# Optimization experiments

Measured on AMD Instinct MI355X. Metric: run time of the kernel, lower is better.

The kernel has to match this reference:

```python
import jax, jax.numpy as jnp
import numpy as np

B, T, IN_DIM, HID = 8, 1024, 32, 512
L = 2                       # num_layers
DI = 2 * HID                # d_inner (expand=2)
DS = 16                     # d_state
K = 4                       # d_conv
DTR = HID // 16             # dt_rank = ceil(d_model/16)
F = 96                      # forecast_len


def setup_inputs() -> dict:
    key = jax.random.key(0)
    ks = jax.random.split(key, 10)
    nrm = lambda k, shape, scale: jax.random.normal(k, shape, jnp.float32) * scale
    x = jax.random.normal(ks[0], (B, T, IN_DIM), jnp.float32)
    ip_w = nrm(ks[1], (HID, IN_DIM), IN_DIM ** -0.5)
    ip_b = jnp.zeros((HID,), jnp.float32)
    norm_w = jnp.ones((L, HID), jnp.float32)
    inp_w = nrm(ks[2], (L, 2 * DI, HID), HID ** -0.5)
    conv_w = nrm(ks[3], (L, DI, 1, K), K ** -0.5)
    conv_b = jnp.zeros((L, DI), jnp.float32)
    xproj_w = nrm(ks[4], (L, DTR + 2 * DS, DI), DI ** -0.5)
    dtproj_w = nrm(ks[5], (L, DI, DTR), DTR ** -0.5)
    dtproj_b = nrm(ks[6], (L, DI), 0.5) - 4.0  # softplus -> small positive dt
    # S4D-real init: A = -[1..d_state], stored as A_log
    A_log = jnp.log(jnp.broadcast_to(jnp.arange(1, DS + 1, dtype=jnp.float32), (L, DI, DS)))
    D = jnp.ones((L, DI), jnp.float32)
    outp_w = nrm(ks[7], (L, HID, DI), DI ** -0.5)
    fc_w = nrm(ks[8], (F, HID), HID ** -0.5)
    fc_b = jnp.zeros((F,), jnp.float32)
    return dict(x=x, ip_w=ip_w, ip_b=ip_b, norm_w=norm_w, inp_w=inp_w,
                conv_w=conv_w, conv_b=conv_b, xproj_w=xproj_w,
                dtproj_w=dtproj_w, dtproj_b=dtproj_b, A_log=A_log, D=D,
                outp_w=outp_w, fc_w=fc_w, fc_b=fc_b)


def _rmsnorm(h, w, eps=1e-5):
    return h * jax.lax.rsqrt(jnp.mean(h * h, axis=-1, keepdims=True) + eps) * w


def _mamba_block(h, inp_w, conv_w, conv_b, xproj_w, dtproj_w, dtproj_b, A_log, Dp, outp_w):
    Bsz = h.shape[0]
    xz = jnp.einsum('btd,ed->bte', h, inp_w)            # (B,T,2*DI)
    x_in, z = jnp.split(xz, 2, axis=-1)
    # causal depthwise conv1d over time
    xc = jnp.transpose(x_in, (0, 2, 1))                 # (B,DI,T)
    xc = jax.lax.conv_general_dilated(
        xc, conv_w, window_strides=(1,), padding=[(K - 1, 0)],
        feature_group_count=DI, dimension_numbers=('NCH', 'OIH', 'NCH'))
    xc = xc + conv_b[None, :, None]
    x_ssm = jax.nn.silu(jnp.transpose(xc, (0, 2, 1)))   # (B,T,DI)
    dbl = jnp.einsum('btd,ed->bte', x_ssm, xproj_w)     # (B,T,DTR+2*DS)
    dt_raw = dbl[..., :DTR]
    Bm = dbl[..., DTR:DTR + DS]                          # (B,T,DS)
    Cm = dbl[..., DTR + DS:]                             # (B,T,DS)
    delta = jax.nn.softplus(jnp.einsum('btr,dr->btd', dt_raw, dtproj_w) + dtproj_b)
    A = -jnp.exp(A_log)                                  # (DI,DS)

    def step(hst, inp):
        dt_t, B_t, C_t, x_t = inp                        # (B,DI),(B,DS),(B,DS),(B,DI)
        dA = jnp.exp(dt_t[:, :, None] * A)               # (B,DI,DS)
        hst = hst * dA + dt_t[:, :, None] * B_t[:, None, :] * x_t[:, :, None]
        y_t = jnp.einsum('bds,bs->bd', hst, C_t)
        return hst, y_t

    h0 = jnp.zeros((Bsz, DI, DS), dtype=h.dtype)
    xs = (jnp.moveaxis(delta, 1, 0), jnp.moveaxis(Bm, 1, 0),
          jnp.moveaxis(Cm, 1, 0), jnp.moveaxis(x_ssm, 1, 0))
    _, ys = jax.lax.scan(step, h0, xs)                   # ys: (T,B,DI)
    y = jnp.moveaxis(ys, 0, 1) + x_ssm * Dp
    y = y * jax.nn.silu(z)
    return jnp.einsum('btd,ed->bte', y, outp_w)


def reference(x, ip_w, ip_b, norm_w, inp_w, conv_w, conv_b, xproj_w,
              dtproj_w, dtproj_b, A_log, D, outp_w, fc_w, fc_b):
    coeff = jnp.array([0.3, 0.5, 0.9, 1.0], dtype=x.dtype)
    x = x.at[:, :, :4].multiply(coeff)
    h = jnp.einsum('bti,hi->bth', x, ip_w) + ip_b        # (B,T,HID)
    for l in range(L):
        h = h + _mamba_block(_rmsnorm(h, norm_w[l]), inp_w[l], conv_w[l],
                             conv_b[l], xproj_w[l], dtproj_w[l], dtproj_b[l],
                             A_log[l], D[l], outp_w[l])
    last = h[:, -1, :]
    return last @ fc_w.T + fc_b                          # (B,F)
```

## Files before the change

### kernel.cpp

```cpp
#include <hip/hip_runtime.h>
#include <math.h>

#define NB   8
#define NT   1024
#define NIN  32
#define NH   512
#define NL   2
#define NDI  1024
#define NDS  16
#define NK   4
#define NDTR 32
#define NF   96
#define NBT  (NB*NT)
#define NE2  (2*NDI)
#define NC   32
#define TC   (NT/NC)

typedef __attribute__((ext_vector_type(8))) short  short8;
typedef __attribute__((ext_vector_type(8))) __bf16 bf16x8;
typedef __attribute__((ext_vector_type(4))) float  f32x4;

__device__ inline void bsplit(float a, short& hi, short& lo) {
  unsigned u = __float_as_uint(a);
  unsigned r = (u + 0x7fffu + ((u >> 16) & 1u)) & 0xffff0000u;
  hi = (short)(r >> 16);
  float res = a - __uint_as_float(r);
  unsigned u2 = __float_as_uint(res);
  lo = (short)((u2 + 0x7fffu + ((u2 >> 16) & 1u)) >> 16);
}

__device__ inline f32x4 mfma_bf16(short8 a, short8 b, f32x4 c) {
  union Cast { short8 s; bf16x8 h; };
  Cast ca, cb; ca.s = a; cb.s = b;
  return __builtin_amdgcn_mfma_f32_16x16x32_bf16(ca.h, cb.h, c, 0, 0, 0);
}

__device__ inline void gld_lds16(const short* g, short* l) {
  __builtin_amdgcn_global_load_lds(
      (const __attribute__((address_space(1))) unsigned int*)g,
      (__attribute__((address_space(3))) unsigned int*)l, 16, 0, 0);
}

__global__ __launch_bounds__(256) void k_input_proj(
    const float* __restrict__ x, const float* __restrict__ ip_w,
    const float* __restrict__ ip_b, float* __restrict__ h) {
  __shared__ float xt[NIN][65];
  __shared__ float wt[NIN][132];
  int tid = threadIdx.x;
  int r0 = blockIdx.x * 64, c0 = blockIdx.y * 128;
  #pragma unroll
  for (int it = 0; it < 2; it++) {
    int i = tid + it*256;
    int row = i >> 3, seg = i & 7;
    float4 v = *(const float4*)&x[(size_t)(r0+row)*NIN + seg*4];
    if (seg == 0) { v.x *= 0.3f; v.y *= 0.5f; v.z *= 0.9f; }
    xt[seg*4+0][row] = v.x; xt[seg*4+1][row] = v.y;
    xt[seg*4+2][row] = v.z; xt[seg*4+3][row] = v.w;
  }
  #pragma unroll
  for (int it = 0; it < 4; it++) {
    int i = tid + it*256;
    int col = i >> 3, seg = i & 7;
    float4 v = *(const float4*)&ip_w[(size_t)(c0+col)*NIN + seg*4];
    wt[seg*4+0][col] = v.x; wt[seg*4+1][col] = v.y;
    wt[seg*4+2][col] = v.z; wt[seg*4+3][col] = v.w;
  }
  __syncthreads();
  int tx = tid & 31, ty = tid >> 5;
  float acc[8][4];
  #pragma unroll
  for (int i = 0; i < 8; i++)
    #pragma unroll
    for (int j = 0; j < 4; j++) acc[i][j] = 0.f;
  #pragma unroll
  for (int k = 0; k < NIN; k++) {
    float4 w4 = *(const float4*)&wt[k][tx*4];
    #pragma unroll
    for (int i = 0; i < 8; i++) {
      float a = xt[k][ty + 8*i];
      acc[i][0] = fmaf(a, w4.x, acc[i][0]);
      acc[i][1] = fmaf(a, w4.y, acc[i][1]);
      acc[i][2] = fmaf(a, w4.z, acc[i][2]);
      acc[i][3] = fmaf(a, w4.w, acc[i][3]);
    }
  }
  float4 bias = *(const float4*)&ip_b[c0 + tx*4];
  #pragma unroll
  for (int i = 0; i < 8; i++) {
    float4 o = make_float4(acc[i][0]+bias.x, acc[i][1]+bias.y,
                           acc[i][2]+bias.z, acc[i][3]+bias.w);
    *(float4*)&h[(size_t)(r0 + ty + 8*i)*NH + c0 + tx*4] = o;
  }
}

__global__ __launch_bounds__(256) void k_rms_split(
    const float* __restrict__ h, const float* __restrict__ nw,
    short* __restrict__ oh, short* __restrict__ ol) {
  int row = blockIdx.x, tid = threadIdx.x;
  float2 v = *(const float2*)&h[(size_t)row*NH + tid*2];
  float ss = v.x*v.x + v.y*v.y;
  #pragma unroll
  for (int off = 32; off > 0; off >>= 1) ss += __shfl_down(ss, off, 64);
  __shared__ float red[4];
  __shared__ float sc_sh;
  if ((tid & 63) == 0) red[tid >> 6] = ss;
  __syncthreads();
  if (tid == 0) sc_sh = rsqrtf((red[0]+red[1]+red[2]+red[3]) * (1.0f/NH) + 1e-5f);
  __syncthreads();
  float sc = sc_sh;
  float2 w2 = *(const float2*)&nw[tid*2];
  short h0,l0,h1,l1;
  bsplit(v.x*sc*w2.x, h0, l0);
  bsplit(v.y*sc*w2.y, h1, l1);
  ushort2 hh; hh.x=(unsigned short)h0; hh.y=(unsigned short)h1;
  ushort2 ll; ll.x=(unsigned short)l0; ll.y=(unsigned short)l1;
  *(ushort2*)&oh[(size_t)row*NH + tid*2] = hh;
  *(ushort2*)&ol[(size_t)row*NH + tid*2] = ll;
}

__global__ __launch_bounds__(256) void k_split_w(
    const float* __restrict__ W, short* __restrict__ wh, short* __restrict__ wl) {
  int i = (blockIdx.x*256 + threadIdx.x) * 8;
  float4 a = *(const float4*)&W[i];
  float4 b = *(const float4*)&W[i+4];
  float v[8] = {a.x,a.y,a.z,a.w,b.x,b.y,b.z,b.w};
  short8 H, L;
  #pragma unroll
  for (int j = 0; j < 8; j++) { short hi, lo; bsplit(v[j], hi, lo); H[j] = hi; L[j] = lo; }
  *(short8*)&wh[i] = H;
  *(short8*)&wl[i] = L;
}

__global__ __launch_bounds__(256) void k_gemm_b3(
    const short* __restrict__ Ah, const short* __restrict__ Al,
    const short* __restrict__ Bh, const short* __restrict__ Bl,
    float* __restrict__ C, int M, int N, int Kd, int accum) {
  __shared__ short lAh[4096], lAl[4096], lBh[4096], lBl[4096];
  int tid = threadIdx.x;
  int lane = tid & 63, w = tid >> 6;
  int m = lane & 15, q = lane >> 4;
  int bm = blockIdx.x * 128, bn = blockIdx.y * 128;
  int wm = (w & 1) * 64, wn = (w >> 1) * 64;
  int s = q ^ ((m >> 1) & 3);
  int ca = ((wm + m) * 4 + s) * 8;
  int cb = ((wn + m) * 4 + s) * 8;

  int r0 = tid >> 2,        s0 = (tid & 3) ^ ((r0 >> 1) & 3);
  int c1 = 256 + tid, r1 = c1 >> 2, s1 = (c1 & 3) ^ ((r1 >> 1) & 3);
  const short* gAh0 = Ah + (size_t)(bm + r0) * Kd + s0 * 8;
  const short* gAh1 = Ah + (size_t)(bm + r1) * Kd + s1 * 8;
  const short* gAl0 = Al + (size_t)(bm + r0) * Kd + s0 * 8;
  const short* gAl1 = Al + (size_t)(bm + r1) * Kd + s1 * 8;
  const short* gBh0 = Bh + (size_t)(bn + r0) * Kd + s0 * 8;
  const short* gBh1 = Bh + (size_t)(bn + r1) * Kd + s1 * 8;
  const short* gBl0 = Bl + (size_t)(bn + r0) * Kd + s0 * 8;
  const short* gBl1 = Bl + (size_t)(bn + r1) * Kd + s1 * 8;
  int ld0 = (tid & ~63) * 8;
  int ld1 = 2048 + ld0;

  f32x4 acc[4][4];
  #pragma unroll
  for (int i = 0; i < 4; i++)
    #pragma unroll
    for (int j = 0; j < 4; j++) acc[i][j] = (f32x4)0.f;

  for (int k0 = 0; k0 < Kd; k0 += 32) {
    __syncthreads();
    gld_lds16(gAh0 + k0, lAh + ld0); gld_lds16(gAh1 + k0, lAh + ld1);
    gld_lds16(gAl0 + k0, lAl + ld0); gld_lds16(gAl1 + k0, lAl + ld1);
    gld_lds16(gBh0 + k0, lBh + ld0); gld_lds16(gBh1 + k0, lBh + ld1);
    gld_lds16(gBl0 + k0, lBl + ld0); gld_lds16(gBl1 + k0, lBl + ld1);
    __syncthreads();
    short8 fAh[4], fAl[4];
    #pragma unroll
    for (int mt = 0; mt < 4; mt++) {
      fAh[mt] = *(const short8*)&lAh[ca + mt*512];
      fAl[mt] = *(const short8*)&lAl[ca + mt*512];
    }
    #pragma unroll
    for (int nt = 0; nt < 4; nt++) {
      short8 fBh = *(const short8*)&lBh[cb + nt*512];
      short8 fBl = *(const short8*)&lBl[cb + nt*512];
      #pragma unroll
      for (int mt = 0; mt < 4; mt++) {
        acc[mt][nt] = mfma_bf16(fAh[mt], fBh, acc[mt][nt]);
        acc[mt][nt] = mfma_bf16(fAl[mt], fBh, acc[mt][nt]);
        acc[mt][nt] = mfma_bf16(fAh[mt], fBl, acc[mt][nt]);
      }
    }
  }
  __syncthreads();
  float* tile = ((float*)lAh) + w * 320;
  int rr = lane >> 2, cc2 = (lane & 3) * 4;
  #pragma unroll
  for (int mt = 0; mt < 4; mt++) {
    #pragma unroll
    for (int nt = 0; nt < 4; nt++) {
      f32x4 v = acc[mt][nt];
      #pragma unroll
      for (int r2 = 0; r2 < 4; r2++) tile[(q*4+r2)*20 + m] = v[r2];
      __builtin_amdgcn_wave_barrier();
      f32x4 o = *(const f32x4*)&tile[rr*20 + cc2];
      __builtin_amdgcn_wave_barrier();
      size_t gi = (size_t)(bm + wm + mt*16 + rr) * N + (bn + wn + nt*16 + cc2);
      if (accum) {
        f32x4 old = *(const f32x4*)&C[gi];
        o.x += old.x; o.y += old.y; o.z += old.z; o.w += old.w;
      }
      *(f32x4*)&C[gi] = o;
    }
  }
}

__global__ __launch_bounds__(256) void k_conv_silu(
    const float* __restrict__ xz, const float* __restrict__ cw,
    const float* __restrict__ cb, float* __restrict__ xs) {
  int idx = blockIdx.x*256 + threadIdx.x;
  int d = idx & (NDI-1);
  int row = idx >> 10;
  int t = row & (NT-1);
  const float* base = xz + (size_t)row*NE2 + d;
  float4 w = *(const float4*)(cw + d*NK);
  float acc = cb[d] + w.w * base[0];
  if (t >= 1) acc += w.z * base[-(ptrdiff_t)NE2];
  if (t >= 2) acc += w.y * base[-2*(ptrdiff_t)NE2];
  if (t >= 3) acc += w.x * base[-3*(ptrdiff_t)NE2];
  xs[idx] = acc / (1.0f + expf(-acc));
}

__global__ __launch_bounds__(256) void k_xproj(
    const float* __restrict__ xs, const float* __restrict__ xw,
    float* __restrict__ dbl) {
  __shared__ float As[64][36];
  __shared__ float Bs[64][68];
  int tid = threadIdx.x;
  int r0 = blockIdx.x * 32;
  int tx = tid & 15, ty = tid >> 4;
  float acc[2][4];
  #pragma unroll
  for (int i = 0; i < 2; i++)
    #pragma unroll
    for (int j = 0; j < 4; j++) acc[i][j] = 0.f;

  for (int k0 = 0; k0 < NDI; k0 += 64) {
    __syncthreads();
    #pragma unroll
    for (int it = 0; it < 2; it++) {
      int i = tid + it*256;
      int row = i >> 4, seg = i & 15;
      float4 v = *(const float4*)&xs[(size_t)(r0+row)*NDI + k0 + seg*4];
      As[seg*4+0][row] = v.x; As[seg*4+1][row] = v.y;
      As[seg*4+2][row] = v.z; As[seg*4+3][row] = v.w;
    }
    #pragma unroll
    for (int it = 0; it < 4; it++) {
      int i = tid + it*256;
      int row = i >> 4, seg = i & 15;
      float4 v = *(const float4*)&xw[(size_t)row*NDI + k0 + seg*4];
      Bs[seg*4+0][row] = v.x; Bs[seg*4+1][row] = v.y;
      Bs[seg*4+2][row] = v.z; Bs[seg*4+3][row] = v.w;
    }
    __syncthreads();
    #pragma unroll
    for (int k = 0; k < 64; k++) {
      float2 a2 = *(const float2*)&As[k][ty*2];
      float4 b4 = *(const float4*)&Bs[k][tx*4];
      acc[0][0]=fmaf(a2.x,b4.x,acc[0][0]); acc[0][1]=fmaf(a2.x,b4.y,acc[0][1]);
      acc[0][2]=fmaf(a2.x,b4.z,acc[0][2]); acc[0][3]=fmaf(a2.x,b4.w,acc[0][3]);
      acc[1][0]=fmaf(a2.y,b4.x,acc[1][0]); acc[1][1]=fmaf(a2.y,b4.y,acc[1][1]);
      acc[1][2]=fmaf(a2.y,b4.z,acc[1][2]); acc[1][3]=fmaf(a2.y,b4.w,acc[1][3]);
    }
  }
  #pragma unroll
  for (int i = 0; i < 2; i++) {
    float4 v = make_float4(acc[i][0], acc[i][1], acc[i][2], acc[i][3]);
    *(float4*)&dbl[(size_t)(r0 + ty*2 + i)*64 + tx*4] = v;
  }
}

__global__ __launch_bounds__(256) void k_dtproj(
    const float* __restrict__ dbl, const float* __restrict__ dtw,
    const float* __restrict__ dtb, float* __restrict__ dly) {
  __shared__ float As[32][68];
  __shared__ float Bs[32][68];
  int tid = threadIdx.x;
  int r0 = blockIdx.x * 64, c0 = blockIdx.y * 64;
  int tx = tid & 15, ty = tid >> 4;
  {
    #pragma unroll
    for (int it = 0; it < 2; it++) {
      int i = tid + it*256;
      int row = i >> 3, seg = i & 7;
      float4 v = *(const float4*)&dbl[(size_t)(r0+row)*64 + seg*4];
      As[seg*4+0][row] = v.x; As[seg*4+1][row] = v.y;
      As[seg*4+2][row] = v.z; As[seg*4+3][row] = v.w;
      float4 u = *(const float4*)&dtw[(size_t)(c0+row)*NDTR + seg*4];
      Bs[seg*4+0][row] = u.x; Bs[seg*4+1][row] = u.y;
      Bs[seg*4+2][row] = u.z; Bs[seg*4+3][row] = u.w;
    }
  }
  __syncthreads();
  float acc[4][4];
  #pragma unroll
  for (int i = 0; i < 4; i++)
    #pragma unroll
    for (int j = 0; j < 4; j++) acc[i][j] = 0.f;
  #pragma unroll
  for (int k = 0; k < 32; k++) {
    float4 a4 = *(const float4*)&As[k][ty*4];
    float4 b4 = *(const float4*)&Bs[k][tx*4];
    acc[0][0]=fmaf(a4.x,b4.x,acc[0][0]); acc[0][1]=fmaf(a4.x,b4.y,acc[0][1]);
    acc[0][2]=fmaf(a4.x,b4.z,acc[0][2]); acc[0][3]=fmaf(a4.x,b4.w,acc[0][3]);
    acc[1][0]=fmaf(a4.y,b4.x,acc[1][0]); acc[1][1]=fmaf(a4.y,b4.y,acc[1][1]);
    acc[1][2]=fmaf(a4.y,b4.z,acc[1][2]); acc[1][3]=fmaf(a4.y,b4.w,acc[1][3]);
    acc[2][0]=fmaf(a4.z,b4.x,acc[2][0]); acc[2][1]=fmaf(a4.z,b4.y,acc[2][1]);
    acc[2][2]=fmaf(a4.z,b4.z,acc[2][2]); acc[2][3]=fmaf(a4.z,b4.w,acc[2][3]);
    acc[3][0]=fmaf(a4.w,b4.x,acc[3][0]); acc[3][1]=fmaf(a4.w,b4.y,acc[3][1]);
    acc[3][2]=fmaf(a4.w,b4.z,acc[3][2]); acc[3][3]=fmaf(a4.w,b4.w,acc[3][3]);
  }
  float4 bias = *(const float4*)&dtb[c0 + tx*4];
  #pragma unroll
  for (int i = 0; i < 4; i++) {
    float v[4] = {acc[i][0]+bias.x, acc[i][1]+bias.y, acc[i][2]+bias.z, acc[i][3]+bias.w};
    float4 o;
    o.x = fmaxf(v[0],0.f) + log1pf(expf(-fabsf(v[0])));
    o.y = fmaxf(v[1],0.f) + log1pf(expf(-fabsf(v[1])));
    o.z = fmaxf(v[2],0.f) + log1pf(expf(-fabsf(v[2])));
    o.w = fmaxf(v[3],0.f) + log1pf(expf(-fabsf(v[3])));
    *(float4*)&dly[(size_t)(r0 + ty*4 + i)*NDI + c0 + tx*4] = o;
  }
}

__global__ __launch_bounds__(256) void k_scan_chunk(
    const float* __restrict__ dly, const float* __restrict__ xs,
    const float* __restrict__ dbl, const float* __restrict__ A_log,
    float* __restrict__ aprod, float* __restrict__ hend) {
  int bx = blockIdx.x;
  int c    = bx & (NC-1);
  int dblk = (bx >> 5) & 3;
  int b    = bx >> 7;
  int d = (dblk << 8) + threadIdx.x;
  float a[NDS], ap[NDS], h[NDS];
  #pragma unroll
  for (int s = 0; s < NDS; s++) {
    a[s] = -expf(A_log[d*NDS + s]);
    ap[s] = 1.f; h[s] = 0.f;
  }
  size_t row0 = (size_t)b*NT + (size_t)c*TC;
  for (int t = 0; t < TC; t++) {
    size_t r = row0 + t;
    float dl = dly[r*NDI + d];
    float xv = xs[r*NDI + d];
    float bc[NDS];
    #pragma unroll
    for (int i = 0; i < NDS; i++) bc[i] = dbl[r*64 + 32 + i];
    float dlx = dl * xv;
    #pragma unroll
    for (int s = 0; s < NDS; s++) {
      float dA = __expf(dl * a[s]);
      ap[s] *= dA;
      h[s] = fmaf(h[s], dA, dlx * bc[s]);
    }
  }
  size_t o = (((size_t)b*NC + c)*NDI + d)*NDS;
  #pragma unroll
  for (int s = 0; s < NDS; s += 4) {
    *(float4*)&aprod[o + s] = make_float4(ap[s], ap[s+1], ap[s+2], ap[s+3]);
    *(float4*)&hend [o + s] = make_float4(h[s],  h[s+1],  h[s+2],  h[s+3]);
  }
}

__global__ __launch_bounds__(256) void k_scan_combine(
    const float* __restrict__ aprod, const float* __restrict__ hend,
    float* __restrict__ hinit) {
  int idx = blockIdx.x*256 + threadIdx.x;
  int b  = idx >> 14;
  int ds = idx & 16383;
  float hcur = 0.f;
  for (int c = 0; c < NC; c++) {
    size_t o = (((size_t)b*NC + c) << 14) + ds;
    hinit[o] = hcur;
    hcur = fmaf(aprod[o], hcur, hend[o]);
  }
}

__global__ __launch_bounds__(256) void k_scan_emit(
    const float* __restrict__ dly, const float* __restrict__ xs,
    const float* __restrict__ xz, const float* __restrict__ dbl,
    const float* __restrict__ A_log, const float* __restrict__ Dp,
    const float* __restrict__ hinit,
    short* __restrict__ yhp, short* __restrict__ ylp) {
  int bx = blockIdx.x;
  int c    = bx & (NC-1);
  int dblk = (bx >> 5) & 3;
  int b    = bx >> 7;
  int d = (dblk << 8) + threadIdx.x;
  float a[NDS], h[NDS];
  size_t o = (((size_t)b*NC + c)*NDI + d)*NDS;
  #pragma unroll
  for (int s = 0; s < NDS; s++) {
    a[s] = -expf(A_log[d*NDS + s]);
    h[s] = hinit[o + s];
  }
  float Dd = Dp[d];
  size_t row0 = (size_t)b*NT + (size_t)c*TC;

  float dl_n = dly[row0*NDI + d];
  float xv_n = xs[row0*NDI + d];
  float zv_n = xz[row0*NE2 + NDI + d];
  for (int t = 0; t < TC; t++) {
    size_t r = row0 + t;
    float dl = dl_n, xv = xv_n, zv = zv_n;
    float bc[32];
    #pragma unroll
    for (int i = 0; i < 32; i++) bc[i] = dbl[r*64 + 32 + i];
    if (t + 1 < TC) {
      dl_n = dly[(r+1)*NDI + d];
      xv_n = xs[(r+1)*NDI + d];
      zv_n = xz[(r+1)*NE2 + NDI + d];
    }
    float dlx = dl * xv;
    float y = 0.f;
    #pragma unroll
    for (int s = 0; s < NDS; s++) {
      float dA = __expf(dl * a[s]);
      h[s] = fmaf(h[s], dA, dlx * bc[s]);
      y = fmaf(h[s], bc[16 + s], y);
    }
    y = (y + xv*Dd) * (zv / (1.0f + __expf(-zv)));
    short yh, yl; bsplit(y, yh, yl);
    yhp[r*NDI + d] = yh;
    ylp[r*NDI + d] = yl;
  }
}

__global__ __launch_bounds__(96) void k_fc(
    const float* __restrict__ h, const float* __restrict__ fc_w,
    const float* __restrict__ fc_b, float* __restrict__ out) {
  int b = blockIdx.x, f = threadIdx.x;
  __shared__ float hr[NH];
  for (int i = f; i < NH; i += NF) hr[i] = h[((size_t)b*NT + (NT-1))*NH + i];
  __syncthreads();
  const float4* wp = (const float4*)(fc_w + (size_t)f*NH);
  float acc = fc_b[f];
  for (int i = 0; i < NH/4; i++) {
    float4 w4 = wp[i];
    acc += hr[i*4+0]*w4.x + hr[i*4+1]*w4.y + hr[i*4+2]*w4.z + hr[i*4+3]*w4.w;
  }
  out[b*NF + f] = acc;
}

extern "C" void kernel_launch(void* const* d_in, const int* in_sizes, int n_in,
                              void* d_out, int out_size, void* d_ws, size_t ws_size,
                              hipStream_t stream) {
  (void)in_sizes; (void)n_in; (void)out_size; (void)ws_size;
  const float* x        = (const float*)d_in[0];
  const float* ip_w     = (const float*)d_in[1];
  const float* ip_b     = (const float*)d_in[2];
  const float* norm_w   = (const float*)d_in[3];
  const float* inp_w    = (const float*)d_in[4];
  const float* conv_w   = (const float*)d_in[5];
  const float* conv_b   = (const float*)d_in[6];
  const float* xproj_w  = (const float*)d_in[7];
  const float* dtproj_w = (const float*)d_in[8];
  const float* dtproj_b = (const float*)d_in[9];
  const float* A_log    = (const float*)d_in[10];
  const float* Dv       = (const float*)d_in[11];
  const float* outp_w   = (const float*)d_in[12];
  const float* fc_w     = (const float*)d_in[13];
  const float* fc_b     = (const float*)d_in[14];
  float* out = (float*)d_out;

  float* ws    = (float*)d_ws;
  float* h     = ws;
  float* xzb   = h     + 4194304;
  float* xs    = xzb   + 16777216;
  float* dblb  = xs    + 8388608;
  float* dly   = dblb  + 524288;
  float* aprod = dly   + 8388608;
  float* hend  = aprod + 4194304;
  float* hinit = hend  + 4194304;
  short* w1h   = (short*)(hinit + 4194304);
  short* w1l   = w1h + 1048576;
  short* w2h   = w1l + 1048576;
  short* w2l   = w2h + 524288;
  short* a1h   = (short*)dly;
  short* a1l   = a1h + 4194304;
  short* yh    = (short*)aprod;
  short* yl    = (short*)hend;

  k_input_proj<<<dim3(NBT/64, NH/128), 256, 0, stream>>>(x, ip_w, ip_b, h);
  for (int l = 0; l < NL; l++) {
    k_rms_split<<<NBT, 256, 0, stream>>>(h, norm_w + l*NH, a1h, a1l);
    k_split_w<<<(NE2*NH)/(256*8), 256, 0, stream>>>(inp_w + (size_t)l*NE2*NH, w1h, w1l);
    k_gemm_b3<<<dim3(NBT/128, NE2/128), 256, 0, stream>>>(
        a1h, a1l, w1h, w1l, xzb, NBT, NE2, NH, 0);
    k_conv_silu<<<(NBT*NDI)/256, 256, 0, stream>>>(
        xzb, conv_w + l*NDI*NK, conv_b + l*NDI, xs);
    k_xproj<<<NBT/32, 256, 0, stream>>>(xs, xproj_w + (size_t)l*64*NDI, dblb);
    k_dtproj<<<dim3(NBT/64, NDI/64), 256, 0, stream>>>(
        dblb, dtproj_w + (size_t)l*NDI*NDTR, dtproj_b + l*NDI, dly);
    k_scan_chunk<<<NB*4*NC, 256, 0, stream>>>(
        dly, xs, dblb, A_log + (size_t)l*NDI*NDS, aprod, hend);
    k_scan_combine<<<(NB*NDI*NDS)/256, 256, 0, stream>>>(aprod, hend, hinit);
    k_scan_emit<<<NB*4*NC, 256, 0, stream>>>(
        dly, xs, xzb, dblb, A_log + (size_t)l*NDI*NDS, Dv + l*NDI, hinit, yh, yl);
    k_split_w<<<(NH*NDI)/(256*8), 256, 0, stream>>>(outp_w + (size_t)l*NH*NDI, w2h, w2l);
    k_gemm_b3<<<dim3(NBT/128, NH/128), 256, 0, stream>>>(
        yh, yl, w2h, w2l, h, NBT, NH, NDI, 1);
  }
  k_fc<<<NB, NF, 0, stream>>>(h, fc_w, fc_b, out);
}
```

Measured before the change: 707.7 us.

## Fuse conv+SiLU into x_proj and recompute dt projection inside scan kernels

The depthwise causal conv and SiLU now run inside the x_proj GEMM kernel, loading a haloed xz tile into shared memory and writing xs as a side output. The separate dt_proj kernel and its 32 MB delta buffer are removed; both scan kernels recompute delta per step from the dt-rank columns of dbl with per-thread dt weights held in registers, plus softplus. Weight splitting for both layers is hoisted out of the layer loop into two launches. This cuts launches and a large activation round trip through memory, at the cost of more register pressure and repeated dt math (done in both scan passes).

```diff
diff --git a/kernel.cpp b/kernel.cpp
--- a/kernel.cpp
+++ b/kernel.cpp
@@ -212,29 +212,16 @@
   }
 }
 
-__global__ __launch_bounds__(256) void k_conv_silu(
+__global__ __launch_bounds__(256) void k_convxproj(
     const float* __restrict__ xz, const float* __restrict__ cw,
-    const float* __restrict__ cb, float* __restrict__ xs) {
-  int idx = blockIdx.x*256 + threadIdx.x;
-  int d = idx & (NDI-1);
-  int row = idx >> 10;
-  int t = row & (NT-1);
-  const float* base = xz + (size_t)row*NE2 + d;
-  float4 w = *(const float4*)(cw + d*NK);
-  float acc = cb[d] + w.w * base[0];
-  if (t >= 1) acc += w.z * base[-(ptrdiff_t)NE2];
-  if (t >= 2) acc += w.y * base[-2*(ptrdiff_t)NE2];
-  if (t >= 3) acc += w.x * base[-3*(ptrdiff_t)NE2];
-  xs[idx] = acc / (1.0f + expf(-acc));
-}
-
-__global__ __launch_bounds__(256) void k_xproj(
-    const float* __restrict__ xs, const float* __restrict__ xw,
-    float* __restrict__ dbl) {
-  __shared__ float As[64][36];
+    const float* __restrict__ cb, const float* __restrict__ xw,
+    float* __restrict__ xs, float* __restrict__ dbl) {
+  __shared__ float xin[35*68];
+  __shared__ float As[64*33];
   __shared__ float Bs[64][68];
   int tid = threadIdx.x;
   int r0 = blockIdx.x * 32;
+  int t0 = r0 & (NT-1);
   int tx = tid & 15, ty = tid >> 4;
   float acc[2][4];
   #pragma unroll
@@ -245,12 +232,15 @@
   for (int k0 = 0; k0 < NDI; k0 += 64) {
     __syncthreads();
     #pragma unroll
-    for (int it = 0; it < 2; it++) {
+    for (int it = 0; it < 3; it++) {
       int i = tid + it*256;
-      int row = i >> 4, seg = i & 15;
-      float4 v = *(const float4*)&xs[(size_t)(r0+row)*NDI + k0 + seg*4];
-      As[seg*4+0][row] = v.x; As[seg*4+1][row] = v.y;
-      As[seg*4+2][row] = v.z; As[seg*4+3][row] = v.w;
+      if (i < 560) {
+        int row = i >> 4, seg = i & 15;
+        float4 v;
+        if (t0 == 0 && row < 3) v = make_float4(0.f, 0.f, 0.f, 0.f);
+        else v = *(const float4*)&xz[(size_t)(r0 - 3 + row)*NE2 + k0 + seg*4];
+        *(float4*)&xin[row*68 + seg*4] = v;
+      }
     }
     #pragma unroll
     for (int it = 0; it < 4; it++) {
@@ -262,13 +252,29 @@
     }
     __syncthreads();
     #pragma unroll
+    for (int it = 0; it < 8; it++) {
+      int i = tid + it*256;
+      int row = i >> 6, c = i & 63;
+      float4 w = *(const float4*)&cw[(k0 + c)*NK];
+      float v = cb[k0 + c]
+              + w.w * xin[(row+3)*68 + c]
+              + w.z * xin[(row+2)*68 + c]
+              + w.y * xin[(row+1)*68 + c]
+              + w.x * xin[(row+0)*68 + c];
+      v = v / (1.0f + expf(-v));
+      As[c*33 + row] = v;
+      xs[(size_t)(r0 + row)*NDI + k0 + c] = v;
+    }
+    __syncthreads();
+    #pragma unroll
     for (int k = 0; k < 64; k++) {
-      float2 a2 = *(const float2*)&As[k][ty*2];
+      float a0 = As[k*33 + ty*2];
+      float a1 = As[k*33 + ty*2 + 1];
       float4 b4 = *(const float4*)&Bs[k][tx*4];
-      acc[0][0]=fmaf(a2.x,b4.x,acc[0][0]); acc[0][1]=fmaf(a2.x,b4.y,acc[0][1]);
-      acc[0][2]=fmaf(a2.x,b4.z,acc[0][2]); acc[0][3]=fmaf(a2.x,b4.w,acc[0][3]);
-      acc[1][0]=fmaf(a2.y,b4.x,acc[1][0]); acc[1][1]=fmaf(a2.y,b4.y,acc[1][1]);
-      acc[1][2]=fmaf(a2.y,b4.z,acc[1][2]); acc[1][3]=fmaf(a2.y,b4.w,acc[1][3]);
+      acc[0][0]=fmaf(a0,b4.x,acc[0][0]); acc[0][1]=fmaf(a0,b4.y,acc[0][1]);
+      acc[0][2]=fmaf(a0,b4.z,acc[0][2]); acc[0][3]=fmaf(a0,b4.w,acc[0][3]);
+      acc[1][0]=fmaf(a1,b4.x,acc[1][0]); acc[1][1]=fmaf(a1,b4.y,acc[1][1]);
+      acc[1][2]=fmaf(a1,b4.z,acc[1][2]); acc[1][3]=fmaf(a1,b4.w,acc[1][3]);
     }
   }
   #pragma unroll
@@ -278,88 +284,44 @@
   }
 }
 
-__global__ __launch_bounds__(256) void k_dtproj(
-    const float* __restrict__ dbl, const float* __restrict__ dtw,
-    const float* __restrict__ dtb, float* __restrict__ dly) {
-  __shared__ float As[32][68];
-  __shared__ float Bs[32][68];
-  int tid = threadIdx.x;
-  int r0 = blockIdx.x * 64, c0 = blockIdx.y * 64;
-  int tx = tid & 15, ty = tid >> 4;
-  {
-    #pragma unroll
-    for (int it = 0; it < 2; it++) {
-      int i = tid + it*256;
-      int row = i >> 3, seg = i & 7;
-      float4 v = *(const float4*)&dbl[(size_t)(r0+row)*64 + seg*4];
-      As[seg*4+0][row] = v.x; As[seg*4+1][row] = v.y;
-      As[seg*4+2][row] = v.z; As[seg*4+3][row] = v.w;
-      float4 u = *(const float4*)&dtw[(size_t)(c0+row)*NDTR + seg*4];
-      Bs[seg*4+0][row] = u.x; Bs[seg*4+1][row] = u.y;
-      Bs[seg*4+2][row] = u.z; Bs[seg*4+3][row] = u.w;
-    }
-  }
-  __syncthreads();
-  float acc[4][4];
-  #pragma unroll
-  for (int i = 0; i < 4; i++)
-    #pragma unroll
-    for (int j = 0; j < 4; j++) acc[i][j] = 0.f;
-  #pragma unroll
-  for (int k = 0; k < 32; k++) {
-    float4 a4 = *(const float4*)&As[k][ty*4];
-    float4 b4 = *(const float4*)&Bs[k][tx*4];
-    acc[0][0]=fmaf(a4.x,b4.x,acc[0][0]); acc[0][1]=fmaf(a4.x,b4.y,acc[0][1]);
-    acc[0][2]=fmaf(a4.x,b4.z,acc[0][2]); acc[0][3]=fmaf(a4.x,b4.w,acc[0][3]);
-    acc[1][0]=fmaf(a4.y,b4.x,acc[1][0]); acc[1][1]=fmaf(a4.y,b4.y,acc[1][1]);
-    acc[1][2]=fmaf(a4.y,b4.z,acc[1][2]); acc[1][3]=fmaf(a4.y,b4.w,acc[1][3]);
-    acc[2][0]=fmaf(a4.z,b4.x,acc[2][0]); acc[2][1]=fmaf(a4.z,b4.y,acc[2][1]);
-    acc[2][2]=fmaf(a4.z,b4.z,acc[2][2]); acc[2][3]=fmaf(a4.z,b4.w,acc[2][3]);
-    acc[3][0]=fmaf(a4.w,b4.x,acc[3][0]); acc[3][1]=fmaf(a4.w,b4.y,acc[3][1]);
-    acc[3][2]=fmaf(a4.w,b4.z,acc[3][2]); acc[3][3]=fmaf(a4.w,b4.w,acc[3][3]);
-  }
-  float4 bias = *(const float4*)&dtb[c0 + tx*4];
-  #pragma unroll
-  for (int i = 0; i < 4; i++) {
-    float v[4] = {acc[i][0]+bias.x, acc[i][1]+bias.y, acc[i][2]+bias.z, acc[i][3]+bias.w};
-    float4 o;
-    o.x = fmaxf(v[0],0.f) + log1pf(expf(-fabsf(v[0])));
-    o.y = fmaxf(v[1],0.f) + log1pf(expf(-fabsf(v[1])));
-    o.z = fmaxf(v[2],0.f) + log1pf(expf(-fabsf(v[2])));
-    o.w = fmaxf(v[3],0.f) + log1pf(expf(-fabsf(v[3])));
-    *(float4*)&dly[(size_t)(r0 + ty*4 + i)*NDI + c0 + tx*4] = o;
-  }
-}
-
 __global__ __launch_bounds__(256) void k_scan_chunk(
-    const float* __restrict__ dly, const float* __restrict__ xs,
-    const float* __restrict__ dbl, const float* __restrict__ A_log,
+    const float* __restrict__ xs, const float* __restrict__ dbl,
+    const float* __restrict__ dtw, const float* __restrict__ dtb,
+    const float* __restrict__ A_log,
     float* __restrict__ aprod, float* __restrict__ hend) {
   int bx = blockIdx.x;
   int c    = bx & (NC-1);
   int dblk = (bx >> 5) & 3;
   int b    = bx >> 7;
   int d = (dblk << 8) + threadIdx.x;
-  float a[NDS], ap[NDS], h[NDS];
+  float a[NDS], ap[NDS], h[NDS], wr[NDTR];
   #pragma unroll
   for (int s = 0; s < NDS; s++) {
     a[s] = -expf(A_log[d*NDS + s]);
     ap[s] = 1.f; h[s] = 0.f;
   }
+  #pragma unroll
+  for (int k = 0; k < NDTR; k++) wr[k] = dtw[d*NDTR + k];
+  float bias = dtb[d];
   size_t row0 = (size_t)b*NT + (size_t)c*TC;
+  float xv_n = xs[row0*NDI + d];
   for (int t = 0; t < TC; t++) {
     size_t r = row0 + t;
-    float dl = dly[r*NDI + d];
-    float xv = xs[r*NDI + d];
-    float bc[NDS];
-    #pragma unroll
-    for (int i = 0; i < NDS; i++) bc[i] = dbl[r*64 + 32 + i];
+    float raw[48];
+    #pragma unroll
+    for (int i = 0; i < 48; i++) raw[i] = dbl[r*64 + i];
+    float xv = xv_n;
+    if (t + 1 < TC) xv_n = xs[(r+1)*NDI + d];
+    float acc = bias;
+    #pragma unroll
+    for (int k = 0; k < NDTR; k++) acc = fmaf(raw[k], wr[k], acc);
+    float dl = fmaxf(acc, 0.f) + log1pf(expf(-fabsf(acc)));
     float dlx = dl * xv;
     #pragma unroll
     for (int s = 0; s < NDS; s++) {
       float dA = __expf(dl * a[s]);
       ap[s] *= dA;
-      h[s] = fmaf(h[s], dA, dlx * bc[s]);
+      h[s] = fmaf(h[s], dA, dlx * raw[32 + s]);
     }
   }
   size_t o = (((size_t)b*NC + c)*NDI + d)*NDS;
@@ -385,8 +347,9 @@
 }
 
 __global__ __launch_bounds__(256) void k_scan_emit(
-    const float* __restrict__ dly, const float* __restrict__ xs,
-    const float* __restrict__ xz, const float* __restrict__ dbl,
+    const float* __restrict__ xs, const float* __restrict__ xz,
+    const float* __restrict__ dbl,
+    const float* __restrict__ dtw, const float* __restrict__ dtb,
     const float* __restrict__ A_log, const float* __restrict__ Dp,
     const float* __restrict__ hinit,
     short* __restrict__ yhp, short* __restrict__ ylp) {
@@ -395,37 +358,42 @@
   int dblk = (bx >> 5) & 3;
   int b    = bx >> 7;
   int d = (dblk << 8) + threadIdx.x;
-  float a[NDS], h[NDS];
+  float a[NDS], h[NDS], wr[NDTR];
   size_t o = (((size_t)b*NC + c)*NDI + d)*NDS;
   #pragma unroll
   for (int s = 0; s < NDS; s++) {
     a[s] = -expf(A_log[d*NDS + s]);
     h[s] = hinit[o + s];
   }
+  #pragma unroll
+  for (int k = 0; k < NDTR; k++) wr[k] = dtw[d*NDTR + k];
+  float bias = dtb[d];
   float Dd = Dp[d];
   size_t row0 = (size_t)b*NT + (size_t)c*TC;
 
-  float dl_n = dly[row0*NDI + d];
   float xv_n = xs[row0*NDI + d];
   float zv_n = xz[row0*NE2 + NDI + d];
   for (int t = 0; t < TC; t++) {
     size_t r = row0 + t;
-    float dl = dl_n, xv = xv_n, zv = zv_n;
-    float bc[32];
-    #pragma unroll
-    for (int i = 0; i < 32; i++) bc[i] = dbl[r*64 + 32 + i];
+    float raw[64];
+    #pragma unroll
+    for (int i = 0; i < 64; i++) raw[i] = dbl[r*64 + i];
+    float xv = xv_n, zv = zv_n;
     if (t + 1 < TC) {
-      dl_n = dly[(r+1)*NDI + d];
       xv_n = xs[(r+1)*NDI + d];
       zv_n = xz[(r+1)*NE2 + NDI + d];
     }
+    float acc = bias;
+    #pragma unroll
+    for (int k = 0; k < NDTR; k++) acc = fmaf(raw[k], wr[k], acc);
+    float dl = fmaxf(acc, 0.f) + log1pf(expf(-fabsf(acc)));
     float dlx = dl * xv;
     float y = 0.f;
     #pragma unroll
     for (int s = 0; s < NDS; s++) {
       float dA = __expf(dl * a[s]);
-      h[s] = fmaf(h[s], dA, dlx * bc[s]);
-      y = fmaf(h[s], bc[16 + s], y);
+      h[s] = fmaf(h[s], dA, dlx * raw[32 + s]);
+      y = fmaf(h[s], raw[48 + s], y);
     }
     y = (y + xv*Dd) * (zv / (1.0f + __expf(-zv)));
     short yh, yl; bsplit(y, yh, yl);
@@ -476,38 +444,39 @@
   float* xzb   = h     + 4194304;
   float* xs    = xzb   + 16777216;
   float* dblb  = xs    + 8388608;
-  float* dly   = dblb  + 524288;
-  float* aprod = dly   + 8388608;
+  float* aprod = dblb  + 524288;
   float* hend  = aprod + 4194304;
   float* hinit = hend  + 4194304;
   short* w1h   = (short*)(hinit + 4194304);
-  short* w1l   = w1h + 1048576;
-  short* w2h   = w1l + 1048576;
-  short* w2l   = w2h + 524288;
-  short* a1h   = (short*)dly;
+  short* w1l   = w1h + 2097152;
+  short* w2h   = w1l + 2097152;
+  short* w2l   = w2h + 1048576;
+  short* a1h   = (short*)aprod;
   short* a1l   = a1h + 4194304;
   short* yh    = (short*)aprod;
   short* yl    = (short*)hend;
 
   k_input_proj<<<dim3(NBT/64, NH/128), 256, 0, stream>>>(x, ip_w, ip_b, h);
+  k_split_w<<<(NL*NE2*NH)/(256*8), 256, 0, stream>>>(inp_w, w1h, w1l);
+  k_split_w<<<(NL*NH*NDI)/(256*8), 256, 0, stream>>>(outp_w, w2h, w2l);
   for (int l = 0; l < NL; l++) {
     k_rms_split<<<NBT, 256, 0, stream>>>(h, norm_w + l*NH, a1h, a1l);
-    k_split_w<<<(NE2*NH)/(256*8), 256, 0, stream>>>(inp_w + (size_t)l*NE2*NH, w1h, w1l);
     k_gemm_b3<<<dim3(NBT/128, NE2/128), 256, 0, stream>>>(
-        a1h, a1l, w1h, w1l, xzb, NBT, NE2, NH, 0);
-    k_conv_silu<<<(NBT*NDI)/256, 256, 0, stream>>>(
-        xzb, conv_w + l*NDI*NK, conv_b + l*NDI, xs);
-    k_xproj<<<NBT/32, 256, 0, stream>>>(xs, xproj_w + (size_t)l*64*NDI, dblb);
-    k_dtproj<<<dim3(NBT/64, NDI/64), 256, 0, stream>>>(
-        dblb, dtproj_w + (size_t)l*NDI*NDTR, dtproj_b + l*NDI, dly);
+        a1h, a1l, w1h + (size_t)l*NE2*NH, w1l + (size_t)l*NE2*NH,
+        xzb, NBT, NE2, NH, 0);
+    k_convxproj<<<NBT/32, 256, 0, stream>>>(
+        xzb, conv_w + l*NDI*NK, conv_b + l*NDI, xproj_w + (size_t)l*64*NDI,
+        xs, dblb);
     k_scan_chunk<<<NB*4*NC, 256, 0, stream>>>(
-        dly, xs, dblb, A_log + (size_t)l*NDI*NDS, aprod, hend);
+        xs, dblb, dtproj_w + (size_t)l*NDI*NDTR, dtproj_b + l*NDI,
+        A_log + (size_t)l*NDI*NDS, aprod, hend);
     k_scan_combine<<<(NB*NDI*NDS)/256, 256, 0, stream>>>(aprod, hend, hinit);
     k_scan_emit<<<NB*4*NC, 256, 0, stream>>>(
-        dly, xs, xzb, dblb, A_log + (size_t)l*NDI*NDS, Dv + l*NDI, hinit, yh, yl);
-    k_split_w<<<(NH*NDI)/(256*8), 256, 0, stream>>>(outp_w + (size_t)l*NH*NDI, w2h, w2l);
+        xs, xzb, dblb, dtproj_w + (size_t)l*NDI*NDTR, dtproj_b + l*NDI,
+        A_log + (size_t)l*NDI*NDS, Dv + l*NDI, hinit, yh, yl);
     k_gemm_b3<<<dim3(NBT/128, NH/128), 256, 0, stream>>>(
-        yh, yl, w2h, w2l, h, NBT, NH, NDI, 1);
+        yh, yl, w2h + (size_t)l*NH*NDI, w2l + (size_t)l*NH*NDI,
+        h, NBT, NH, NDI, 1);
   }
   k_fc<<<NB, NF, 0, stream>>>(h, fc_w, fc_b, out);
 }
```

Result: slower. 743.0 us (+5.0%).
